# Optimization experiments

Measured on AMD Instinct MI355X. Metric: run time of the kernel, lower is better.

The kernel has to match this reference:

```python
import jax, jax.numpy as jnp
import numpy as np
import math

HEADS = 8

def setup_inputs() -> dict:
    key = jax.random.key(0)
    k1, k2 = jax.random.split(key)
    B, C, H, W = 8, 512, 32, 32
    x = jax.random.normal(k1, (B, C, H, W), dtype=jnp.float32)
    # weight-norm 1x1 conv params: v ~ N(0, 0.05), g initialized to ||v|| (torch weight_norm default)
    proj_v = jax.random.normal(k2, (3 * C, C), dtype=jnp.float32) * 0.05
    proj_g = jnp.linalg.norm(proj_v, axis=1)
    proj_b = jnp.zeros((3 * C,), dtype=jnp.float32)
    return {"x": x, "proj_v": proj_v, "proj_g": proj_g, "proj_b": proj_b}

def reference(x, proj_v, proj_g, proj_b):
    B, C, H, W = x.shape
    heads = HEADS
    dim = C // heads
    N = H * W
    # weight-normalized 1x1 conv: w = g * v / ||v|| per output channel
    w = proj_g[:, None] * proj_v / jnp.linalg.norm(proj_v, axis=1, keepdims=True)
    c = jnp.einsum('oc,bchw->bohw', w, x) + proj_b[None, :, None, None]
    c = c.reshape(B, 3, heads, dim, N)
    q, k, v = c[:, 0], c[:, 1], c[:, 2]  # each (B, heads, dim, N)
    scale = 1.0 / math.sqrt(dim)
    attn = jnp.einsum('bhdq,bhdk->bhqk', q, k) * scale  # (B, heads, N, N)
    attn = jax.nn.softmax(attn, axis=-1)
    out = jnp.einsum('bhdk,bhqk->bhdq', v, attn)  # (B, heads, dim, N)
    return x + out.reshape(B, C, H, W)
```

## Files before the change

### kernel.cpp

```cpp
#include <hip/hip_runtime.h>

typedef _Float16 f16;
typedef _Float16 f16x2 __attribute__((ext_vector_type(2)));
typedef _Float16 f16x4 __attribute__((ext_vector_type(4)));
typedef _Float16 f16x8 __attribute__((ext_vector_type(8)));
typedef float f32x4 __attribute__((ext_vector_type(4)));
typedef float f32x16 __attribute__((ext_vector_type(16)));
typedef unsigned int u32;
typedef unsigned int u32x4 __attribute__((ext_vector_type(4)));

__device__ inline f32x16 mfma32(f16x8 a, f16x8 b, f32x16 c) {
    return __builtin_amdgcn_mfma_f32_32x32x16_f16(a, b, c, 0, 0, 0);
}

__device__ inline u32 pk2u(float a, float b) {
    return __builtin_bit_cast(u32, __builtin_amdgcn_cvt_pkrtz(a, b));
}

__device__ inline void gl16(const f16* g, f16* l) {
    __builtin_amdgcn_global_load_lds(
        (const __attribute__((address_space(1))) void*)g,
        (__attribute__((address_space(3))) void*)l, 16, 0, 0);
}

__device__ inline void st8(f16* p, f16x8 v) {
    *(f16x4*)p = __builtin_shufflevector(v, v, 0, 1, 2, 3);
    *(f16x4*)(p + 4) = __builtin_shufflevector(v, v, 4, 5, 6, 7);
}
__device__ inline f16x8 ld8(const f16* p) {
    f16x4 lo = *(const f16x4*)p;
    f16x4 hi = *(const f16x4*)(p + 4);
    return __builtin_shufflevector(lo, hi, 0, 1, 2, 3, 4, 5, 6, 7);
}

__global__ __launch_bounds__(256) void prep_k(const float* __restrict__ pv,
                                              const float* __restrict__ pg,
                                              f16* __restrict__ w,
                                              const float* __restrict__ x,
                                              f16* __restrict__ xT) {
    int bid = blockIdx.x;
    if (bid < 1536) {
        int o = bid;
        const float* row = pv + (size_t)o * 512;
        float s = 0.f;
        for (int c = threadIdx.x; c < 512; c += 256) { float t = row[c]; s += t * t; }
        for (int off = 32; off; off >>= 1) s += __shfl_down(s, off, 64);
        __shared__ float red[4];
        int lane = threadIdx.x & 63, wid = threadIdx.x >> 6;
        if (lane == 0) red[wid] = s;
        __syncthreads();
        float tot = red[0] + red[1] + red[2] + red[3];
        float scale = pg[o] * rsqrtf(tot);
        for (int c = threadIdx.x; c < 512; c += 256)
            w[(size_t)o * 512 + c] = (f16)(row[c] * scale);
    } else {
        int t2 = bid - 1536;
        int n0 = (t2 & 31) * 32, c0 = ((t2 >> 5) & 15) * 32, b = t2 >> 9;
        int tx = threadIdx.x & 31, ty = threadIdx.x >> 5;
        __shared__ float t[32][33];
        const float* xb = x + (size_t)b * 512 * 1024;
        for (int i = 0; i < 4; i++)
            t[ty + 8 * i][tx] = xb[(size_t)(c0 + ty + 8 * i) * 1024 + n0 + tx];
        __syncthreads();
        f16* xTb = xT + (size_t)b * 1024 * 512;
        for (int i = 0; i < 4; i++)
            xTb[(size_t)(n0 + ty + 8 * i) * 512 + c0 + tx] = (f16)t[tx][ty + 8 * i];
    }
}

__global__ __launch_bounds__(256) void qkv_gemm_k(const f16* __restrict__ w,
                                                  const f16* __restrict__ xT,
                                                  const float* __restrict__ pb,
                                                  f16* __restrict__ qk,
                                                  f16* __restrict__ v) {
    __shared__ f16 lA[128 * 64];
    __shared__ f16 lB[128 * 64];
    int b = blockIdx.z;
    int oBase = blockIdx.y * 128;
    int nBase = blockIdx.x * 128;
    const f16* xb = xT + (size_t)b * 1024 * 512;
    int tid = threadIdx.x, lane = tid & 63, warp = tid >> 6;
    int wy = warp >> 1, wx = warp & 1;
    int l31 = lane & 31, hi = lane >> 5;

    int srow = lane >> 3;
    int phys = lane & 7;
    int schunk = phys ^ srow;
    const f16* aS[4]; const f16* bS[4]; f16* dA[4]; f16* dB[4];
    for (int j = 0; j < 4; j++) {
        int rb = (warp * 4 + j) * 8;
        aS[j] = w  + (size_t)(oBase + rb + srow) * 512 + schunk * 8;
        bS[j] = xb + (size_t)(nBase + rb + srow) * 512 + schunk * 8;
        dA[j] = &lA[rb * 64];
        dB[j] = &lB[rb * 64];
    }
    int phk[4];
    for (int ks = 0; ks < 4; ks++)
        phk[ks] = (((ks * 2 + hi) ^ (l31 & 7))) * 8;

    f32x16 acc[2][2] = {};

    for (int i = 0; i < 8; i++) {
        int k0 = i * 64;
        __syncthreads();
        for (int j = 0; j < 4; j++) {
            gl16(aS[j] + k0, dA[j]);
            gl16(bS[j] + k0, dB[j]);
        }
        __syncthreads();
        for (int ks = 0; ks < 4; ks++) {
            f16x8 af[2], bf[2];
            for (int mi = 0; mi < 2; mi++)
                af[mi] = *(f16x8*)&lA[(wy * 64 + mi * 32 + l31) * 64 + phk[ks]];
            for (int ni = 0; ni < 2; ni++)
                bf[ni] = *(f16x8*)&lB[(wx * 64 + ni * 32 + l31) * 64 + phk[ks]];
            for (int mi = 0; mi < 2; mi++)
                for (int ni = 0; ni < 2; ni++)
                    acc[mi][ni] = mfma32(af[mi], bf[ni], acc[mi][ni]);
        }
    }

    int selB = oBase >> 9;
    for (int mi = 0; mi < 2; mi++) {
        for (int g = 0; g < 4; g++) {
            int oR = oBase + wy * 64 + mi * 32 + 8 * g + 4 * hi;
            int h = (oR >> 6) & 7, d0 = oR & 63;
            for (int ni = 0; ni < 2; ni++) {
                int n = nBase + wx * 64 + ni * 32 + l31;
                if (selB < 2) {
                    float sc = selB == 0 ? 0.125f : 1.0f;
                    f16x4 o4;
                    for (int r = 0; r < 4; r++)
                        o4[r] = (f16)((acc[mi][ni][g * 4 + r] + pb[oR + r]) * sc);
                    *(f16x4*)&qk[((((size_t)b * 2 + selB) * 8 + h) * 1024 + n) * 64 + d0] = o4;
                } else {
                    for (int r = 0; r < 4; r++) {
                        float val = acc[mi][ni][g * 4 + r] + pb[oR + r];
                        v[(((size_t)b * 8 + h) * 64 + d0 + r) * 1024 + n] = (f16)val;
                    }
                }
            }
        }
    }
}

#define ALDK 68
__global__ __launch_bounds__(256, 2) void attn_k(const f16* __restrict__ qk,
                                                 const f16* __restrict__ vg,
                                                 const float* __restrict__ x,
                                                 float* __restrict__ out) {
    __shared__ __align__(16) f16 smem[2 * 64 * ALDK];
    f16* lK = smem;
    f16* lV = smem + 64 * ALDK;

    int bh = blockIdx.y;
    int b = bh >> 3, h = bh & 7;
    int qBase = blockIdx.x * 128;
    int tid = threadIdx.x, lane = tid & 63, warp = tid >> 6;
    int l31 = lane & 31, hi = lane >> 5;

    const f16* qbase = qk + (((size_t)b * 2 + 0) * 8 + h) * 1024 * 64;
    const f16* kbase = qk + (((size_t)b * 2 + 1) * 8 + h) * 1024 * 64;
    const f16* vbase = vg + ((size_t)b * 8 + h) * 64 * 1024;

    int q0 = qBase + warp * 32;
    f16x8 aq[4];
    for (int ks = 0; ks < 4; ks++)
        aq[ks] = *(const f16x8*)&qbase[(size_t)(q0 + l31) * 64 + ks * 16 + hi * 8];

    int sr0 = tid >> 3, sc0 = (tid & 7) * 8;
    int sr1 = sr0 + 32;

    f16x8 rK[2], rV[2];
    rK[0] = *(const f16x8*)&kbase[(size_t)sr0 * 64 + sc0];
    rK[1] = *(const f16x8*)&kbase[(size_t)sr1 * 64 + sc0];
    rV[0] = *(const f16x8*)&vbase[(size_t)sr0 * 1024 + sc0];
    rV[1] = *(const f16x8*)&vbase[(size_t)sr1 * 1024 + sc0];

    f32x16 accO[2] = {};
    float l_acc = 0.f;

    for (int kt = 0; kt < 16; kt++) {
        __syncthreads();
        st8(&lK[sr0 * ALDK + sc0], rK[0]);
        st8(&lK[sr1 * ALDK + sc0], rK[1]);
        st8(&lV[sr0 * ALDK + sc0], rV[0]);
        st8(&lV[sr1 * ALDK + sc0], rV[1]);
        __syncthreads();
        if (kt < 15) {
            const f16* kb = kbase + (size_t)(kt + 1) * 64 * 64;
            rK[0] = *(const f16x8*)&kb[(size_t)sr0 * 64 + sc0];
            rK[1] = *(const f16x8*)&kb[(size_t)sr1 * 64 + sc0];
            rV[0] = *(const f16x8*)&vbase[(size_t)sr0 * 1024 + (kt + 1) * 64 + sc0];
            rV[1] = *(const f16x8*)&vbase[(size_t)sr1 * 1024 + (kt + 1) * 64 + sc0];
        }

        u32 P0[2][4], P1[2][4];
        float rs = 0.f;
        for (int mt = 0; mt < 2; mt++) {
            f16x8 ak[4];
            for (int ks = 0; ks < 4; ks++)
                ak[ks] = ld8(&lK[(mt * 32 + l31) * ALDK + ks * 16 + hi * 8]);
            f32x16 stt = {};
            for (int ks = 0; ks < 4; ks++)
                stt = mfma32(ak[ks], aq[ks], stt);
            for (int g = 0; g < 4; g++) {
                float p0 = __expf(stt[g * 4 + 0]);
                float p1 = __expf(stt[g * 4 + 1]);
                float p2 = __expf(stt[g * 4 + 2]);
                float p3 = __expf(stt[g * 4 + 3]);
                rs += (p0 + p1) + (p2 + p3);
                P0[mt][g] = pk2u(p0, p1);
                P1[mt][g] = pk2u(p2, p3);
            }
        }
        l_acc += rs;

        f16x8 av[2][4];
        for (int dt = 0; dt < 2; dt++)
            for (int ks = 0; ks < 4; ks++)
                av[dt][ks] = ld8(&lV[(dt * 32 + l31) * ALDK + ks * 16 + hi * 8]);
        f16x8 bfrag[4];
        for (int ks = 0; ks < 4; ks++) {
            int mt = ks >> 1, ge = 2 * (ks & 1);
            u32 e00 = P0[mt][ge], e01 = P0[mt][ge + 1];
            u32 e10 = P1[mt][ge], e11 = P1[mt][ge + 1];
            u32 k0 = hi ? e01 : e00;
            u32 k1 = hi ? e11 : e10;
            u32 s0 = hi ? e00 : e01;
            u32 s1 = hi ? e10 : e11;
            u32 r0 = __shfl_xor(s0, 32, 64);
            u32 r1 = __shfl_xor(s1, 32, 64);
            u32 a0 = hi ? r0 : k0, a1 = hi ? r1 : k1;
            u32 b0 = hi ? k0 : r0, b1 = hi ? k1 : r1;
            u32x4 t = {a0, a1, b0, b1};
            bfrag[ks] = __builtin_bit_cast(f16x8, t);
        }
        for (int dt = 0; dt < 2; dt++)
            for (int ks = 0; ks < 4; ks++)
                accO[dt] = mfma32(av[dt][ks], bfrag[ks], accO[dt]);
    }

    float lt = l_acc + __shfl_xor(l_acc, 32, 64);
    float rl = 1.0f / lt;
    int q = q0 + l31;
    for (int dt = 0; dt < 2; dt++)
        for (int g = 0; g < 4; g++)
            for (int r = 0; r < 4; r++) {
                int d = dt * 32 + 8 * g + 4 * hi + r;
                size_t gi = ((size_t)b * 512 + h * 64 + d) * 1024 + q;
                out[gi] = x[gi] + accO[dt][g * 4 + r] * rl;
            }
}

extern "C" void kernel_launch(void* const* d_in, const int* in_sizes, int n_in,
                              void* d_out, int out_size, void* d_ws, size_t ws_size,
                              hipStream_t stream) {
    (void)in_sizes; (void)n_in; (void)out_size; (void)ws_size;
    const float* x  = (const float*)d_in[0];
    const float* pv = (const float*)d_in[1];
    const float* pg = (const float*)d_in[2];
    const float* pb = (const float*)d_in[3];
    float* out = (float*)d_out;

    char* ws = (char*)d_ws;
    f16* w   = (f16*)(ws);
    f16* xT  = (f16*)(ws + 1572864);
    f16* qk  = (f16*)(ws + 1572864 + 8388608);
    f16* v   = (f16*)(ws + 1572864 + 8388608 + 16777216);

    hipLaunchKernelGGL(prep_k,     dim3(5632),     dim3(256), 0, stream, pv, pg, w, x, xT);
    hipLaunchKernelGGL(qkv_gemm_k, dim3(8, 12, 8), dim3(256), 0, stream, w, xT, pb, qk, v);
    hipLaunchKernelGGL(attn_k,     dim3(8, 64),    dim3(256), 0, stream, qk, v, x, out);
}
```

Measured before the change: 129.4 us.

## Double-buffer K/V tiles via direct global-to-LDS loads with XOR swizzle

Replaces the register-staged K/V tile loads (global→register→LDS with a padded stride) with asynchronous global_load_lds into a double-buffered LDS area. The LDS layout drops the padding and uses an XOR swizzle on 16-byte chunks, so 128-bit ds_reads can be used without bank conflicts. The goal is to overlap the next tile's fetch with the current tile's compute, remove the register round trip, and drop one barrier per iteration. LDS use doubles to 32 KB per block, which may limit occupancy. Correctness depends on the async-load completion waits placed around the single barrier.

```diff
diff --git a/kernel.cpp b/kernel.cpp
--- a/kernel.cpp
+++ b/kernel.cpp
@@ -21,16 +21,6 @@
     __builtin_amdgcn_global_load_lds(
         (const __attribute__((address_space(1))) void*)g,
         (__attribute__((address_space(3))) void*)l, 16, 0, 0);
-}
-
-__device__ inline void st8(f16* p, f16x8 v) {
-    *(f16x4*)p = __builtin_shufflevector(v, v, 0, 1, 2, 3);
-    *(f16x4*)(p + 4) = __builtin_shufflevector(v, v, 4, 5, 6, 7);
-}
-__device__ inline f16x8 ld8(const f16* p) {
-    f16x4 lo = *(const f16x4*)p;
-    f16x4 hi = *(const f16x4*)(p + 4);
-    return __builtin_shufflevector(lo, hi, 0, 1, 2, 3, 4, 5, 6, 7);
 }
 
 __global__ __launch_bounds__(256) void prep_k(const float* __restrict__ pv,
@@ -144,15 +134,13 @@
     }
 }
 
-#define ALDK 68
+#define TSZ 4096
+
 __global__ __launch_bounds__(256, 2) void attn_k(const f16* __restrict__ qk,
                                                  const f16* __restrict__ vg,
                                                  const float* __restrict__ x,
                                                  float* __restrict__ out) {
-    __shared__ __align__(16) f16 smem[2 * 64 * ALDK];
-    f16* lK = smem;
-    f16* lV = smem + 64 * ALDK;
-
+    __shared__ __align__(16) f16 smem[4 * TSZ];
     int bh = blockIdx.y;
     int b = bh >> 3, h = bh & 7;
     int qBase = blockIdx.x * 128;
@@ -168,39 +156,42 @@
     for (int ks = 0; ks < 4; ks++)
         aq[ks] = *(const f16x8*)&qbase[(size_t)(q0 + l31) * 64 + ks * 16 + hi * 8];
 
-    int sr0 = tid >> 3, sc0 = (tid & 7) * 8;
-    int sr1 = sr0 + 32;
-
-    f16x8 rK[2], rV[2];
-    rK[0] = *(const f16x8*)&kbase[(size_t)sr0 * 64 + sc0];
-    rK[1] = *(const f16x8*)&kbase[(size_t)sr1 * 64 + sc0];
-    rV[0] = *(const f16x8*)&vbase[(size_t)sr0 * 1024 + sc0];
-    rV[1] = *(const f16x8*)&vbase[(size_t)sr1 * 1024 + sc0];
+    int rb = lane >> 3;
+    int gchunk = (lane & 7) ^ rb;
+    const f16* kS0 = kbase + (size_t)(warp * 8 + rb) * 64 + gchunk * 8;
+    const f16* vS0 = vbase + (size_t)(warp * 8 + rb) * 1024 + gchunk * 8;
 
     f32x16 accO[2] = {};
     float l_acc = 0.f;
 
+#define STAGE(BUF, KT)                                                        \
+    do {                                                                      \
+        f16* lb = smem + (BUF) * 2 * TSZ;                                     \
+        const f16* ks_ = kS0 + (size_t)(KT) * 4096;                           \
+        const f16* vs_ = vS0 + (size_t)(KT) * 64;                             \
+        gl16(ks_,             lb + warp * 512);                               \
+        gl16(ks_ + 32 * 64,   lb + 2048 + warp * 512);                        \
+        gl16(vs_,             lb + TSZ + warp * 512);                         \
+        gl16(vs_ + 32 * 1024, lb + TSZ + 2048 + warp * 512);                  \
+    } while (0)
+
+    STAGE(0, 0);
+    __syncthreads();
+
     for (int kt = 0; kt < 16; kt++) {
-        __syncthreads();
-        st8(&lK[sr0 * ALDK + sc0], rK[0]);
-        st8(&lK[sr1 * ALDK + sc0], rK[1]);
-        st8(&lV[sr0 * ALDK + sc0], rV[0]);
-        st8(&lV[sr1 * ALDK + sc0], rV[1]);
-        __syncthreads();
-        if (kt < 15) {
-            const f16* kb = kbase + (size_t)(kt + 1) * 64 * 64;
-            rK[0] = *(const f16x8*)&kb[(size_t)sr0 * 64 + sc0];
-            rK[1] = *(const f16x8*)&kb[(size_t)sr1 * 64 + sc0];
-            rV[0] = *(const f16x8*)&vbase[(size_t)sr0 * 1024 + (kt + 1) * 64 + sc0];
-            rV[1] = *(const f16x8*)&vbase[(size_t)sr1 * 1024 + (kt + 1) * 64 + sc0];
-        }
+        int cur = kt & 1;
+        if (kt < 15) STAGE(cur ^ 1, kt + 1);
+        const f16* lK = smem + cur * 2 * TSZ;
+        const f16* lV = lK + TSZ;
 
         u32 P0[2][4], P1[2][4];
         float rs = 0.f;
         for (int mt = 0; mt < 2; mt++) {
             f16x8 ak[4];
-            for (int ks = 0; ks < 4; ks++)
-                ak[ks] = ld8(&lK[(mt * 32 + l31) * ALDK + ks * 16 + hi * 8]);
+            for (int ks = 0; ks < 4; ks++) {
+                int row = mt * 32 + l31;
+                ak[ks] = *(const f16x8*)&lK[row * 64 + (((ks * 2 + hi) ^ (l31 & 7)) << 3)];
+            }
             f32x16 stt = {};
             for (int ks = 0; ks < 4; ks++)
                 stt = mfma32(ak[ks], aq[ks], stt);
@@ -218,8 +209,10 @@
 
         f16x8 av[2][4];
         for (int dt = 0; dt < 2; dt++)
-            for (int ks = 0; ks < 4; ks++)
-                av[dt][ks] = ld8(&lV[(dt * 32 + l31) * ALDK + ks * 16 + hi * 8]);
+            for (int ks = 0; ks < 4; ks++) {
+                int row = dt * 32 + l31;
+                av[dt][ks] = *(const f16x8*)&lV[row * 64 + (((ks * 2 + hi) ^ (l31 & 7)) << 3)];
+            }
         f16x8 bfrag[4];
         for (int ks = 0; ks < 4; ks++) {
             int mt = ks >> 1, ge = 2 * (ks & 1);
@@ -239,7 +232,10 @@
         for (int dt = 0; dt < 2; dt++)
             for (int ks = 0; ks < 4; ks++)
                 accO[dt] = mfma32(av[dt][ks], bfrag[ks], accO[dt]);
-    }
+
+        __syncthreads();
+    }
+#undef STAGE
 
     float lt = l_acc + __shfl_xor(l_acc, 32, 64);
     float rl = 1.0f / lt;
```

Measured after the change: 129.0 us, median of 2. No clear change (-0.3%).
